# Kernel optimization log

Measured on AMD Instinct MI355X. Metric: run time of the kernel, lower is better.

The kernel has to match this reference:

```python
import jax, jax.numpy as jnp
import numpy as np

EPS = 1e-6  # F.normalize eps

N, C, H, W = 2, 64, 64, 64
HEADS, DK, DV = 2, 64, 32


def setup_inputs() -> dict:
    key = jax.random.key(0)
    ks = jax.random.split(key, 9)
    w = lambda k, sh: jax.random.normal(k, sh, jnp.float32) * 0.05
    return {
        "x":  jax.random.normal(ks[0], (N, C, H, W), jnp.float32),
        "Wq": w(ks[1], (HEADS, DK, C)), "bq": w(ks[2], (HEADS, DK)),
        "Wk": w(ks[3], (HEADS, DK, C)), "bk": w(ks[4], (HEADS, DK)),
        "Wv": w(ks[5], (HEADS, DV, C)), "bv": w(ks[6], (HEADS, DV)),
        "Wm": w(ks[7], (C, HEADS * DV)), "bm": w(ks[8], (C,)),
    }


def _l2norm(t):
    # F.normalize(dim=1) on [N, dk, L]; here heads are stacked: [N, h, dk, L], axis=2
    n = jnp.linalg.norm(t, axis=2, keepdims=True)
    return t / jnp.maximum(n, EPS)


def reference(x, Wq, bq, Wk, bk, Wv, bv, Wm, bm):
    n, c, h, w = x.shape
    L = h * w
    xf = x.reshape(n, c, L)  # 1x1 conv == pointwise channel GEMM; x_enc = x (no pos enc)
    Q = jnp.einsum('hkc,ncl->nhkl', Wq, xf) + bq[None, :, :, None]
    K = jnp.einsum('hkc,ncl->nhkl', Wk, xf) + bk[None, :, :, None]
    V = jnp.einsum('hvc,ncl->nhvl', Wv, xf) + bv[None, :, :, None]
    Q = _l2norm(Q)
    K = _l2norm(K)
    # cosine-similarity attention: contract over dk, softmax over keys
    A = jax.nn.softmax(jnp.einsum('nhkl,nhkm->nhlm', Q, K), axis=-1)  # [n,h,L,L]
    R = jnp.einsum('nhlm,nhvm->nhvl', A, V)  # [n,h,dv,L]
    Rc = R.reshape(n, -1, L)  # concat heads along channels
    out = jnp.einsum('oc,ncl->nol', Wm, Rc) + bm[None, :, None]
    return out.reshape(n, c, h, w) + x  # residual
```

## Files before the change

### kernel.cpp

```cpp
#include <hip/hip_runtime.h>
#include <cmath>


typedef __bf16 bf16x8 __attribute__((ext_vector_type(8)));
typedef __bf16 bf16x4 __attribute__((ext_vector_type(4)));
typedef float f4_t __attribute__((ext_vector_type(4)));

#define LQ 4096
#define NH 4
#define KS 8

__device__ inline f4_t mfma16(bf16x8 a, bf16x8 b, f4_t c) {
    return __builtin_amdgcn_mfma_f32_16x16x32_bf16(a, b, c, 0, 0, 0);
}

__device__ inline bf16x8 cvt8(const float* p) {
    f4_t a = *(const f4_t*)p, b = *(const f4_t*)(p + 4);
    bf16x8 r;
    r[0] = (__bf16)a[0]; r[1] = (__bf16)a[1]; r[2] = (__bf16)a[2]; r[3] = (__bf16)a[3];
    r[4] = (__bf16)b[0]; r[5] = (__bf16)b[1]; r[6] = (__bf16)b[2]; r[7] = (__bf16)b[3];
    return r;
}

__global__ __launch_bounds__(256) void k1_qkv(
        const float* __restrict__ x,
        const float* __restrict__ Wq, const float* __restrict__ bq,
        const float* __restrict__ Wk, const float* __restrict__ bk,
        const float* __restrict__ Wv, const float* __restrict__ bv,
        __bf16* __restrict__ Qb, __bf16* __restrict__ Kb,
        __bf16* __restrict__ Vtb) {
    const int tid  = threadIdx.x;
    const int lane = tid & 63;
    const int w    = tid >> 6;
    const int quad = lane >> 4;
    const int l15  = lane & 15;
    const int lt   = blockIdx.x;
    const int n    = blockIdx.y;
    const int l0   = lt * 32;

    __shared__ __bf16 xl[32][72];

    {
        const int c0 = tid >> 5, l = tid & 31;
#pragma unroll
        for (int i = 0; i < 8; ++i) {
            const int c = c0 + i * 8;
            xl[l][c] = (__bf16)x[((size_t)n * 64 + c) * LQ + l0 + l];
        }
    }

    const float* Wqk = (w < 2) ? Wq : Wk;
    const float* bqk = (w < 2) ? bq : bk;
    const int h = w & 1;

    bf16x8 af[4][2], av[2];
#pragma unroll
    for (int t = 0; t < 4; ++t)
#pragma unroll
        for (int kh = 0; kh < 2; ++kh)
            af[t][kh] = cvt8(Wqk + (size_t)(h * 64 + t * 16 + l15) * 64
                                  + kh * 32 + quad * 8);
#pragma unroll
    for (int kh = 0; kh < 2; ++kh)
        av[kh] = cvt8(Wv + (size_t)(w * 16 + l15) * 64 + kh * 32 + quad * 8);

    f4_t binit[4], bvinit;
#pragma unroll
    for (int t = 0; t < 4; ++t)
#pragma unroll
        for (int r = 0; r < 4; ++r)
            binit[t][r] = bqk[h * 64 + t * 16 + quad * 4 + r];
#pragma unroll
    for (int r = 0; r < 4; ++r)
        bvinit[r] = bv[w * 16 + quad * 4 + r];

    __syncthreads();

    f4_t acc[4][2], vacc[2];
#pragma unroll
    for (int lsub = 0; lsub < 2; ++lsub) {
        bf16x8 bf0 = *(const bf16x8*)&xl[lsub * 16 + l15][quad * 8];
        bf16x8 bf1 = *(const bf16x8*)&xl[lsub * 16 + l15][32 + quad * 8];
#pragma unroll
        for (int t = 0; t < 4; ++t) {
            f4_t a = mfma16(af[t][0], bf0, binit[t]);
            acc[t][lsub] = mfma16(af[t][1], bf1, a);
        }
        f4_t va = mfma16(av[0], bf0, bvinit);
        vacc[lsub] = mfma16(av[1], bf1, va);
    }

    const int nh = n * 2 + h;
    __bf16* dst  = (w < 2) ? Qb : Kb;
    const float post = (w < 2) ? 1.44269504f : 1.0f;
#pragma unroll
    for (int lsub = 0; lsub < 2; ++lsub) {
        float ss = 0.f;
#pragma unroll
        for (int t = 0; t < 4; ++t)
#pragma unroll
            for (int r = 0; r < 4; ++r)
                ss = fmaf(acc[t][lsub][r], acc[t][lsub][r], ss);
        ss += __shfl_xor(ss, 16, 64);
        ss += __shfl_xor(ss, 32, 64);
        const float rn = post / fmaxf(sqrtf(ss), 1e-6f);

        const int l = l0 + lsub * 16 + l15;
#pragma unroll
        for (int t = 0; t < 4; ++t) {
            bf16x4 pk;
#pragma unroll
            for (int r = 0; r < 4; ++r) pk[r] = (__bf16)(acc[t][lsub][r] * rn);
            const int kc = t * 2 + (quad >> 1);
            *(bf16x4*)(dst + ((size_t)(nh * 8 + kc) * LQ + l) * 8 + (quad & 1) * 4) = pk;
        }
#pragma unroll
        for (int r = 0; r < 4; ++r) {
            const int vrow = w * 16 + quad * 4 + r;
            Vtb[(size_t)(n * 64 + vrow) * LQ + l] = (__bf16)vacc[lsub][r];
        }
    }
}

__global__ __launch_bounds__(256, 4) void k2_attn(
        const __bf16* __restrict__ Qb, const __bf16* __restrict__ Kb,
        const __bf16* __restrict__ Vtb,
        __bf16* __restrict__ numPb, float* __restrict__ denP) {
    const int tid  = threadIdx.x;
    const int lane = tid & 63;
    const int wave = tid >> 6;
    const int quad = lane >> 4;
    const int l15  = lane & 15;
    const int nh   = blockIdx.y;
    const int ks   = blockIdx.z;
    const int qbase = blockIdx.x * 128 + wave * 32;
    const int kbase = ks * 512;

    __shared__ __bf16 Kl[2][4096];
    __shared__ __bf16 P[4][2][16][72];

    const f4_t fzero = {0.f, 0.f, 0.f, 0.f};

    const __bf16* s_src0, * s_src1;
    {
        const int s0 = tid, s1 = tid + 256;
        const int kc0 = ((s0 >> 6) & 1) * 4 + ((s0 >> 4) & 3);
        const int ll0 = (s0 >> 7) * 16 + (s0 & 15);
        const int kc1 = ((s1 >> 6) & 1) * 4 + ((s1 >> 4) & 3);
        const int ll1 = (s1 >> 7) * 16 + (s1 & 15);
        s_src0 = Kb + ((size_t)(nh * 8 + kc0) * LQ + kbase + ll0) * 8;
        s_src1 = Kb + ((size_t)(nh * 8 + kc1) * LQ + kbase + ll1) * 8;
    }

    bf16x8 qf[2][2];
#pragma unroll
    for (int qt = 0; qt < 2; ++qt)
#pragma unroll
        for (int kh = 0; kh < 2; ++kh)
            qf[qt][kh] = *(const bf16x8*)(Qb +
                ((size_t)(nh * 8 + kh * 4 + quad) * LQ + qbase + qt * 16 + l15) * 8);

    f4_t racc[2][2];
#pragma unroll
    for (int a = 0; a < 2; ++a)
#pragma unroll
        for (int b = 0; b < 2; ++b) racc[a][b] = fzero;
    float den[2] = {0.f, 0.f};

    const __bf16* v_src = Vtb + (size_t)(nh * 32 + l15) * LQ + kbase + quad * 8;

    *(bf16x8*)&Kl[0][(size_t)tid * 8]         = *(const bf16x8*)s_src0;
    *(bf16x8*)&Kl[0][(size_t)(tid + 256) * 8] = *(const bf16x8*)s_src1;
    __syncthreads();

#pragma unroll 2
    for (int ch = 0; ch < 8; ++ch) {
        const int cur = ch & 1;

        if (ch < 7) {
            *(bf16x8*)&Kl[cur ^ 1][(size_t)tid * 8] =
                *(const bf16x8*)(s_src0 + (size_t)(ch + 1) * 512);
            *(bf16x8*)&Kl[cur ^ 1][(size_t)(tid + 256) * 8] =
                *(const bf16x8*)(s_src1 + (size_t)(ch + 1) * 512);
        }

        bf16x8 vf[2][2];
#pragma unroll
        for (int vt = 0; vt < 2; ++vt)
#pragma unroll
            for (int kp = 0; kp < 2; ++kp)
                vf[vt][kp] = *(const bf16x8*)(v_src + (size_t)vt * 16 * LQ
                                              + ch * 64 + kp * 32);

#pragma unroll
        for (int ktp = 0; ktp < 2; ++ktp) {
            bf16x8 kf[2][2];
#pragma unroll
            for (int i = 0; i < 2; ++i)
#pragma unroll
                for (int kh = 0; kh < 2; ++kh)
                    kf[i][kh] = *(const bf16x8*)
                        &Kl[cur][(size_t)((ktp * 2 + i) * 128 + kh * 64
                                          + quad * 16 + l15) * 8];

            f4_t s[2][2];
#pragma unroll
            for (int qt = 0; qt < 2; ++qt)
#pragma unroll
                for (int i = 0; i < 2; ++i) {
                    f4_t t = mfma16(kf[i][0], qf[qt][0], fzero);
                    s[qt][i] = mfma16(kf[i][1], qf[qt][1], t);
                }

#pragma unroll
            for (int qt = 0; qt < 2; ++qt)
#pragma unroll
                for (int i = 0; i < 2; ++i) {
                    bf16x4 pv;
                    float d = 0.f;
#pragma unroll
                    for (int r = 0; r < 4; ++r) {
                        float p = __builtin_exp2f(s[qt][i][r]);
                        d += p;
                        pv[r] = (__bf16)p;
                    }
                    den[qt] += d;
                    *(bf16x4*)&P[wave][qt][l15][(ktp * 2 + i) * 16 + quad * 4] = pv;
                }
        }

#pragma unroll
        for (int qt = 0; qt < 2; ++qt)
#pragma unroll
            for (int kp = 0; kp < 2; ++kp) {
                bf16x8 pf = *(const bf16x8*)&P[wave][qt][l15][kp * 32 + quad * 8];
                racc[0][qt] = mfma16(vf[0][kp], pf, racc[0][qt]);
                racc[1][qt] = mfma16(vf[1][kp], pf, racc[1][qt]);
            }

        __syncthreads();
    }

#pragma unroll
    for (int qt = 0; qt < 2; ++qt) {
        den[qt] += __shfl_xor(den[qt], 16, 64);
        den[qt] += __shfl_xor(den[qt], 32, 64);
    }

    const size_t pb = (size_t)(nh * KS + ks) * LQ;
#pragma unroll
    for (int vt = 0; vt < 2; ++vt)
#pragma unroll
        for (int qt = 0; qt < 2; ++qt) {
            bf16x4 pk;
#pragma unroll
            for (int r = 0; r < 4; ++r) pk[r] = (__bf16)racc[vt][qt][r];
            *(bf16x4*)(numPb + (pb + qbase + qt * 16 + l15) * 32
                             + vt * 16 + quad * 4) = pk;
        }

    if (lane < 16)
#pragma unroll
        for (int qt = 0; qt < 2; ++qt)
            denP[pb + qbase + qt * 16 + lane] = den[qt];
}

__global__ __launch_bounds__(256) void k3_out(
        const __bf16* __restrict__ numPb, const float* __restrict__ denP,
        const float* __restrict__ Wm, const float* __restrict__ bm,
        const float* __restrict__ x, float* __restrict__ out) {
    const int tid = threadIdx.x;
    const int lt  = blockIdx.x;
    const int n   = blockIdx.y;
    const int l0  = lt * 16;

    __shared__ float Rf[64][17];
    __shared__ float dinv[2][16];

    if (tid < 32) {
        const int hh = tid >> 4, li = tid & 15;
        float s = 0.f;
#pragma unroll
        for (int k = 0; k < KS; ++k)
            s += denP[(size_t)((n * 2 + hh) * KS + k) * LQ + l0 + li];
        dinv[hh][li] = 1.0f / s;
    }

    {
        const int v = tid & 31, lg = tid >> 5;
        const int hh = lg & 1, lofs = lg >> 1;
        const size_t base = (size_t)(n * 2 + hh) * KS * LQ;
#pragma unroll
        for (int i = 0; i < 4; ++i) {
            const int l = lofs + 4 * i;
            float s = 0.f;
#pragma unroll
            for (int k = 0; k < KS; ++k)
                s += (float)numPb[(base + (size_t)k * LQ + l0 + l) * 32 + v];
            Rf[hh * 32 + v][l] = s;
        }
    }
    __syncthreads();

    const int l = tid & 15, og = tid >> 4;
    const float d0 = dinv[0][l], d1 = dinv[1][l];
    float rj[64];
#pragma unroll
    for (int j = 0; j < 64; ++j)
        rj[j] = Rf[j][l] * (j < 32 ? d0 : d1);

#pragma unroll
    for (int oi = 0; oi < 4; ++oi) {
        const int o = og * 4 + oi;
        const float* wr = Wm + (size_t)o * 64;
        float a = bm[o];
#pragma unroll
        for (int j4 = 0; j4 < 16; ++j4) {
            f4_t t = *(const f4_t*)(wr + j4 * 4);
            a = fmaf(t[0], rj[j4 * 4 + 0], a);
            a = fmaf(t[1], rj[j4 * 4 + 1], a);
            a = fmaf(t[2], rj[j4 * 4 + 2], a);
            a = fmaf(t[3], rj[j4 * 4 + 3], a);
        }
        const size_t idx = (size_t)(n * 64 + o) * LQ + l0 + l;
        out[idx] = a + x[idx];
    }
}

extern "C" void kernel_launch(void* const* d_in, const int* in_sizes, int n_in,
                              void* d_out, int out_size, void* d_ws, size_t ws_size,
                              hipStream_t stream) {
    const float* x  = (const float*)d_in[0];
    const float* Wq = (const float*)d_in[1];
    const float* bq = (const float*)d_in[2];
    const float* Wk = (const float*)d_in[3];
    const float* bk = (const float*)d_in[4];
    const float* Wv = (const float*)d_in[5];
    const float* bv = (const float*)d_in[6];
    const float* Wm = (const float*)d_in[7];
    const float* bm = (const float*)d_in[8];
    float* out = (float*)d_out;

    __bf16* Qb    = (__bf16*)d_ws;
    __bf16* Kb    = Qb + (size_t)NH * LQ * 64;
    __bf16* Vtb   = Kb + (size_t)NH * LQ * 64;
    __bf16* numPb = Vtb + (size_t)NH * 32 * LQ;
    float*  denP  = (float*)(numPb + (size_t)NH * KS * LQ * 32);

    k1_qkv<<<dim3(128, 2), dim3(256), 0, stream>>>(x, Wq, bq, Wk, bk, Wv, bv,
                                                   Qb, Kb, Vtb);
    k2_attn<<<dim3(32, NH, KS), dim3(256), 0, stream>>>(Qb, Kb, Vtb, numPb, denP);
    k3_out<<<dim3(256, 2), dim3(256), 0, stream>>>(numPb, denP, Wm, bm, x, out);
}
```

Baseline: 112.6 us.

## Load K fragments directly into registers and vectorize partial-sum reduction

The attention kernel stops staging K tiles through double-buffered shared memory with per-chunk barriers. Each lane now loads its MFMA K operand straight from global memory into registers, ping-ponging between two register sets, and the V loads are issued after the first QK MFMAs. The output kernel reads the split-K partial numerators as 8-wide bf16 vectors, sums them in two halves, and combines the halves through shared memory. This removes LDS traffic and block-wide syncs at the cost of more registers and of each wave redundantly fetching K from global/L2.

```diff
diff --git a/kernel.cpp b/kernel.cpp
--- a/kernel.cpp
+++ b/kernel.cpp
@@ -136,21 +136,9 @@
     const int qbase = blockIdx.x * 128 + wave * 32;
     const int kbase = ks * 512;
 
-    __shared__ __bf16 Kl[2][4096];
     __shared__ __bf16 P[4][2][16][72];
 
     const f4_t fzero = {0.f, 0.f, 0.f, 0.f};
-
-    const __bf16* s_src0, * s_src1;
-    {
-        const int s0 = tid, s1 = tid + 256;
-        const int kc0 = ((s0 >> 6) & 1) * 4 + ((s0 >> 4) & 3);
-        const int ll0 = (s0 >> 7) * 16 + (s0 & 15);
-        const int kc1 = ((s1 >> 6) & 1) * 4 + ((s1 >> 4) & 3);
-        const int ll1 = (s1 >> 7) * 16 + (s1 & 15);
-        s_src0 = Kb + ((size_t)(nh * 8 + kc0) * LQ + kbase + ll0) * 8;
-        s_src1 = Kb + ((size_t)(nh * 8 + kc1) * LQ + kbase + ll1) * 8;
-    }
 
     bf16x8 qf[2][2];
 #pragma unroll
@@ -167,55 +155,53 @@
         for (int b = 0; b < 2; ++b) racc[a][b] = fzero;
     float den[2] = {0.f, 0.f};
 
+    const __bf16* k_src0 = Kb + ((size_t)(nh * 8 + quad) * LQ + kbase + l15) * 8;
+    const __bf16* k_src1 = Kb + ((size_t)(nh * 8 + 4 + quad) * LQ + kbase + l15) * 8;
     const __bf16* v_src = Vtb + (size_t)(nh * 32 + l15) * LQ + kbase + quad * 8;
 
-    *(bf16x8*)&Kl[0][(size_t)tid * 8]         = *(const bf16x8*)s_src0;
-    *(bf16x8*)&Kl[0][(size_t)(tid + 256) * 8] = *(const bf16x8*)s_src1;
-    __syncthreads();
-
-#pragma unroll 2
-    for (int ch = 0; ch < 8; ++ch) {
-        const int cur = ch & 1;
-
+    bf16x8 kA[4][2], kB[4][2];
+#pragma unroll
+    for (int kt = 0; kt < 4; ++kt) {
+        kA[kt][0] = *(const bf16x8*)(k_src0 + (size_t)(kt * 16) * 8);
+        kA[kt][1] = *(const bf16x8*)(k_src1 + (size_t)(kt * 16) * 8);
+    }
+
+    auto step = [&](int ch, bf16x8 (&cur)[4][2], bf16x8 (&nxt)[4][2]) {
         if (ch < 7) {
-            *(bf16x8*)&Kl[cur ^ 1][(size_t)tid * 8] =
-                *(const bf16x8*)(s_src0 + (size_t)(ch + 1) * 512);
-            *(bf16x8*)&Kl[cur ^ 1][(size_t)(tid + 256) * 8] =
-                *(const bf16x8*)(s_src1 + (size_t)(ch + 1) * 512);
+#pragma unroll
+            for (int kt = 0; kt < 4; ++kt) {
+                nxt[kt][0] = *(const bf16x8*)(k_src0 +
+                                (size_t)((ch + 1) * 64 + kt * 16) * 8);
+                nxt[kt][1] = *(const bf16x8*)(k_src1 +
+                                (size_t)((ch + 1) * 64 + kt * 16) * 8);
+            }
         }
 
         bf16x8 vf[2][2];
 #pragma unroll
-        for (int vt = 0; vt < 2; ++vt)
-#pragma unroll
-            for (int kp = 0; kp < 2; ++kp)
-                vf[vt][kp] = *(const bf16x8*)(v_src + (size_t)vt * 16 * LQ
-                                              + ch * 64 + kp * 32);
-
-#pragma unroll
-        for (int ktp = 0; ktp < 2; ++ktp) {
-            bf16x8 kf[2][2];
-#pragma unroll
-            for (int i = 0; i < 2; ++i)
-#pragma unroll
-                for (int kh = 0; kh < 2; ++kh)
-                    kf[i][kh] = *(const bf16x8*)
-                        &Kl[cur][(size_t)((ktp * 2 + i) * 128 + kh * 64
-                                          + quad * 16 + l15) * 8];
-
+        for (int pair = 0; pair < 2; ++pair) {
             f4_t s[2][2];
 #pragma unroll
             for (int qt = 0; qt < 2; ++qt)
 #pragma unroll
                 for (int i = 0; i < 2; ++i) {
-                    f4_t t = mfma16(kf[i][0], qf[qt][0], fzero);
-                    s[qt][i] = mfma16(kf[i][1], qf[qt][1], t);
+                    const int kt = pair * 2 + i;
+                    f4_t t = mfma16(cur[kt][0], qf[qt][0], fzero);
+                    s[qt][i] = mfma16(cur[kt][1], qf[qt][1], t);
                 }
-
+            if (pair == 0) {
+#pragma unroll
+                for (int vt = 0; vt < 2; ++vt)
+#pragma unroll
+                    for (int kp = 0; kp < 2; ++kp)
+                        vf[vt][kp] = *(const bf16x8*)(v_src +
+                            (size_t)vt * 16 * LQ + ch * 64 + kp * 32);
+            }
 #pragma unroll
             for (int qt = 0; qt < 2; ++qt)
 #pragma unroll
                 for (int i = 0; i < 2; ++i) {
+                    const int kt = pair * 2 + i;
                     bf16x4 pv;
                     float d = 0.f;
 #pragma unroll
@@ -225,7 +211,7 @@
                         pv[r] = (__bf16)p;
                     }
                     den[qt] += d;
-                    *(bf16x4*)&P[wave][qt][l15][(ktp * 2 + i) * 16 + quad * 4] = pv;
+                    *(bf16x4*)&P[wave][qt][l15][kt * 16 + quad * 4] = pv;
                 }
         }
 
@@ -237,8 +223,11 @@
                 racc[0][qt] = mfma16(vf[0][kp], pf, racc[0][qt]);
                 racc[1][qt] = mfma16(vf[1][kp], pf, racc[1][qt]);
             }
-
-        __syncthreads();
+    };
+
+    for (int ch = 0; ch < 8; ch += 2) {
+        step(ch,     kA, kB);
+        step(ch + 1, kB, kA);
     }
 
 #pragma unroll
@@ -274,7 +263,7 @@
     const int n   = blockIdx.y;
     const int l0  = lt * 16;
 
-    __shared__ float Rf[64][17];
+    __shared__ float Rps[2][64][17];
     __shared__ float dinv[2][16];
 
     if (tid < 32) {
@@ -287,18 +276,21 @@
     }
 
     {
-        const int v = tid & 31, lg = tid >> 5;
-        const int hh = lg & 1, lofs = lg >> 1;
+        const int vg = tid & 3, l = (tid >> 2) & 15;
+        const int hh = (tid >> 6) & 1, sh = tid >> 7;
         const size_t base = (size_t)(n * 2 + hh) * KS * LQ;
-#pragma unroll
-        for (int i = 0; i < 4; ++i) {
-            const int l = lofs + 4 * i;
-            float s = 0.f;
-#pragma unroll
-            for (int k = 0; k < KS; ++k)
-                s += (float)numPb[(base + (size_t)k * LQ + l0 + l) * 32 + v];
-            Rf[hh * 32 + v][l] = s;
-        }
+        float a[8] = {0.f, 0.f, 0.f, 0.f, 0.f, 0.f, 0.f, 0.f};
+#pragma unroll
+        for (int k = 0; k < 4; ++k) {
+            const int kk = sh * 4 + k;
+            bf16x8 v8 = *(const bf16x8*)(numPb +
+                (base + (size_t)kk * LQ + l0 + l) * 32 + vg * 8);
+#pragma unroll
+            for (int j = 0; j < 8; ++j) a[j] += (float)v8[j];
+        }
+#pragma unroll
+        for (int j = 0; j < 8; ++j)
+            Rps[sh][hh * 32 + vg * 8 + j][l] = a[j];
     }
     __syncthreads();
 
@@ -307,7 +299,7 @@
     float rj[64];
 #pragma unroll
     for (int j = 0; j < 64; ++j)
-        rj[j] = Rf[j][l] * (j < 32 ? d0 : d1);
+        rj[j] = (Rps[0][j][l] + Rps[1][j][l]) * (j < 32 ? d0 : d1);
 
 #pragma unroll
     for (int oi = 0; oi < 4; ++oi) {
```

New measurement: 133.9 us. 1.19x slower.
